# Kernel tuning notes

Hardware: AMD Instinct MI355X
Metric: run time of the kernel (lower is better)

The kernel has to match this reference:

```python
import jax, jax.numpy as jnp
import numpy as np

T = 10.0           # distillation temperature (init arg T)
LOSS_WEIGHT = 1.0  # module-level loss_weight (init arg)
EPS_STD = 1e-07
EPS_RATIO = 1e-08

ROWS, BINS = 1048576, 17  # (4*N, n+1), n = 16


def setup_inputs() -> dict:
    key = jax.random.key(0)
    k1, k2, k3 = jax.random.split(key, 3)
    pred = jax.random.normal(k1, (ROWS, BINS), dtype=jnp.float32)
    soft_label = jax.random.normal(k2, (ROWS, BINS), dtype=jnp.float32)
    weight = jax.random.uniform(k3, (ROWS,), dtype=jnp.float32)
    return {"pred": pred, "soft_label": soft_label, "weight": weight}


def _normalize(logit):
    # torch .std() is unbiased (ddof=1)
    mean = jnp.mean(logit, axis=-1, keepdims=True)
    stdv = jnp.std(logit, axis=-1, keepdims=True, ddof=1)
    return (logit - mean) / (EPS_STD + stdv)


def reference(pred, soft_label, weight):
    soft = jax.lax.stop_gradient(soft_label)  # detach_target=True

    # kd_loss_ls with logit_stand=True
    ls = _normalize(pred)
    lt = _normalize(soft)
    log_p_student = jax.nn.log_softmax(ls / T, axis=1)
    log_p_teacher = jax.nn.log_softmax(lt / T, axis=1)
    p_teacher = jnp.exp(log_p_teacher)
    # F.kl_div(log_pred, target, 'none') = target * (log(target) - log_pred)
    loss_ls = jnp.mean(jnp.sum(p_teacher * (log_p_teacher - log_p_student), axis=1)) * (T * T)

    # sum_distributions_loop on target = softmax(soft_label) -- batched full conv1d
    target = jax.nn.softmax(soft, axis=1)            # (4N, bins)
    n_rows, bins = target.shape
    N = n_rows // 4
    t = target.reshape(N, 4, bins)
    top, bottom, left, right = t[:, 0], t[:, 1], t[:, 2], t[:, 3]
    # pad+flip+conv1d in torch == true full convolution, length 2*bins-1 = 2n+1
    conv_full = jax.vmap(lambda a, b: jnp.convolve(a, b, mode='full'))
    sum_lr = conv_full(left, right)                   # (N, 2n+1)
    sum_tb = conv_full(top, bottom)                   # (N, 2n+1)
    target_ratio = sum_lr / (sum_tb + EPS_RATIO)

    # weighted_loss wrapper: loss * weight, then 'mean' reduction; outer * loss_weight
    loss = LOSS_WEIGHT * jnp.mean(loss_ls * weight)
    return loss, target_ratio
```

## Files before the change

kernel.cpp:

```cpp
#include <hip/hip_runtime.h>

#define ROWS 1048576
#define BINS 17
#define RPB 128
#define NBLK (ROWS / RPB)
#define NPART (2 * NBLK)
#define GPB (RPB / 4)
#define CONV_N 33
#define L2E 1.442695040888963f
#define LN2 0.6931471805599453f

template <bool PART>
__global__ __launch_bounds__(128, 4) void kd_main(
    const float* __restrict__ pred,
    const float* __restrict__ soft,
    const float* __restrict__ weight,
    float* __restrict__ out,
    float* __restrict__ ws)
{
    __shared__ float sA[RPB * BINS];
    __shared__ float sB[RPB * BINS];
    const int tid = threadIdx.x;
    const long long base = (long long)blockIdx.x * (RPB * BINS);

    const float4* p4 = reinterpret_cast<const float4*>(pred + base);
    const float4* q4 = reinterpret_cast<const float4*>(soft + base);
    float4* a4 = reinterpret_cast<float4*>(sA);
    float4* b4 = reinterpret_cast<float4*>(sB);
#pragma unroll
    for (int k = 0; k < 4; ++k) {
        a4[k * RPB + tid] = p4[k * RPB + tid];
        b4[k * RPB + tid] = q4[k * RPB + tid];
    }
    if (tid < 32) {
        a4[512 + tid] = p4[512 + tid];
        b4[512 + tid] = q4[512 + tid];
    }
    const float w = weight[blockIdx.x * RPB + tid];
    __syncthreads();

    float x[BINS], y[BINS];
    float sx = 0.f, sy = 0.f, sxx = 0.f, syy = 0.f;
    float xmx = -1e30f, ymx = -1e30f;
#pragma unroll
    for (int j = 0; j < BINS; ++j) {
        x[j] = sA[tid * BINS + j];
        y[j] = sB[tid * BINS + j];
        sx += x[j]; sxx = fmaf(x[j], x[j], sxx); xmx = fmaxf(xmx, x[j]);
        sy += y[j]; syy = fmaf(y[j], y[j], syy); ymx = fmaxf(ymx, y[j]);
    }
    const float mx = sx * (1.0f / BINS);
    const float my = sy * (1.0f / BINS);
    const float vx = fmaxf(fmaf(-sx, mx, sxx), 0.f) * (1.0f / (BINS - 1));
    const float vy = fmaxf(fmaf(-sy, my, syy), 0.f) * (1.0f / (BINS - 1));
    const float sxl = (0.1f * L2E) *
        __builtin_amdgcn_rcpf(1e-7f + __builtin_amdgcn_sqrtf(vx));
    const float syl = (0.1f * L2E) *
        __builtin_amdgcn_rcpf(1e-7f + __builtin_amdgcn_sqrtf(vy));
    const float cA = -xmx * sxl;
    const float cB = -ymx * syl;
    const float cT = -ymx * L2E;

    float et[BINS];
    float sea = 0.f, seb = 0.f, ts = 0.f, sdb = 0.f;
#pragma unroll
    for (int j = 0; j < BINS; ++j) {
        const float aj = fmaf(x[j], sxl, cA);
        const float bj = fmaf(y[j], syl, cB);
        const float ea = exp2f(aj);
        const float eb = exp2f(bj);
        const float tv = exp2f(fmaf(y[j], L2E, cT));
        sea += ea; seb += eb; ts += tv;
        sdb = fmaf(eb, bj - aj, sdb);
        et[j] = tv;
    }
    const float kl = LN2 * (sdb * __builtin_amdgcn_rcpf(seb)
                            + (__log2f(sea) - __log2f(seb)));
    const float invts = __builtin_amdgcn_rcpf(ts);

#pragma unroll
    for (int j = 0; j < BINS; ++j)
        sA[tid * BINS + j] = et[j] * invts;

    float k2 = kl, w2 = w;
#pragma unroll
    for (int off = 32; off >= 1; off >>= 1) {
        k2 += __shfl_down(k2, off, 64);
        w2 += __shfl_down(w2, off, 64);
    }
    if ((tid & 63) == 0) {
        const int wv = tid >> 6;
        if (PART) {
            ws[2 * blockIdx.x + wv]         = k2;
            ws[NPART + 2 * blockIdx.x + wv] = w2;
        } else {
            atomicAdd(&ws[0], k2);
            atomicAdd(&ws[1], w2);
        }
    }

    __syncthreads();

    float* sR = sB;

    if (tid < 64) {
        const int g = tid >> 1;
        const int R = 4 * g + ((tid & 1) ? 0 : 2);
        float f[2 * BINS];
        const float2* pr = reinterpret_cast<const float2*>(&sA[R * BINS]);
#pragma unroll
        for (int i = 0; i < BINS; ++i) {
            const float2 v = pr[i];
            f[2 * i] = v.x; f[2 * i + 1] = v.y;
        }
        float accv[CONV_N];
#pragma unroll
        for (int j = 0; j < CONV_N; ++j) accv[j] = 0.f;
#pragma unroll
        for (int k = 0; k < BINS; ++k)
#pragma unroll
            for (int m = 0; m < BINS; ++m)
                accv[k + m] = fmaf(f[k], f[BINS + m], accv[k + m]);

#pragma unroll
        for (int j = 0; j < CONV_N; ++j) {
            const float o = __shfl_down(accv[j], 1, 64);
            if ((tid & 1) == 0)
                sR[g * CONV_N + j] = accv[j] *
                    __builtin_amdgcn_rcpf(o + 1e-8f);
        }
    }
    __syncthreads();

    const long long ob = 1 + (long long)blockIdx.x * (GPB * CONV_N);
#pragma unroll
    for (int i = 0; i < 8; ++i)
        out[ob + i * RPB + tid] = sR[i * RPB + tid];
    if (tid < 32) out[ob + 1024 + tid] = sR[1024 + tid];
}

template <bool PART>
__global__ __launch_bounds__(1024) void kd_reduce(
    const float* __restrict__ ws, float* __restrict__ out)
{
    if (!PART) {
        if (threadIdx.x == 0)
            out[0] = 100.0f * (ws[0] * (1.0f / ROWS)) * (ws[1] * (1.0f / ROWS));
        return;
    }
    __shared__ float red[32];
    const int tid = threadIdx.x;
    const float4* k4 = reinterpret_cast<const float4*>(ws);
    const float4* w4 = reinterpret_cast<const float4*>(ws + NPART);
    float ks = 0.f, wsum = 0.f;
#pragma unroll
    for (int i = 0; i < 4; ++i) {
        const float4 a = k4[i * 1024 + tid];
        const float4 b = w4[i * 1024 + tid];
        ks += (a.x + a.y) + (a.z + a.w);
        wsum += (b.x + b.y) + (b.z + b.w);
    }
#pragma unroll
    for (int off = 32; off >= 1; off >>= 1) {
        ks += __shfl_down(ks, off, 64);
        wsum += __shfl_down(wsum, off, 64);
    }
    if ((tid & 63) == 0) {
        red[(tid >> 6) * 2 + 0] = ks;
        red[(tid >> 6) * 2 + 1] = wsum;
    }
    __syncthreads();
    if (tid == 0) {
        float K = 0.f, W = 0.f;
#pragma unroll
        for (int i = 0; i < 16; ++i) { K += red[2 * i]; W += red[2 * i + 1]; }
        out[0] = 100.0f * (K * (1.0f / ROWS)) * (W * (1.0f / ROWS));
    }
}

extern "C" void kernel_launch(void* const* d_in, const int* in_sizes, int n_in,
                              void* d_out, int out_size, void* d_ws, size_t ws_size,
                              hipStream_t stream)
{
    const float* pred   = (const float*)d_in[0];
    const float* soft   = (const float*)d_in[1];
    const float* weight = (const float*)d_in[2];
    float* out = (float*)d_out;
    float* ws  = (float*)d_ws;

    if (ws_size >= (size_t)(2 * NPART) * sizeof(float)) {
        kd_main<true><<<NBLK, RPB, 0, stream>>>(pred, soft, weight, out, ws);
        kd_reduce<true><<<1, 1024, 0, stream>>>(ws, out);
    } else {
        hipMemsetAsync(ws, 0, 2 * sizeof(float), stream);
        kd_main<false><<<NBLK, RPB, 0, stream>>>(pred, soft, weight, out, ws);
        kd_reduce<false><<<1, 1024, 0, stream>>>(ws, out);
    }
}
```

Baseline: 183.0 us.

## Load rows directly into registers, drop input LDS staging, raise occupancy

Each thread now reads its 17-float pred and soft rows straight from global memory into registers, replacing the block-wide float4 copy into two shared arrays and the barrier after it. LDS use drops to one array plus a per-row reciprocal slot, and the launch bound is raised to 8 blocks per CU. The softmax normalization of the teacher row is moved into the convolution phase through the stored reciprocal, and the output staging now reuses the same array. The aim is to cut LDS traffic and footprint and to allow more blocks per CU. The trade-off is that the per-thread loads are strided and only 4-byte aligned, so they may not vectorize or coalesce as well as the old float4 copy.

```diff
diff --git a/kernel.cpp b/kernel.cpp
--- a/kernel.cpp
+++ b/kernel.cpp
@@ -11,41 +11,31 @@
 #define LN2 0.6931471805599453f
 
 template <bool PART>
-__global__ __launch_bounds__(128, 4) void kd_main(
+__global__ __launch_bounds__(128, 8) void kd_main(
     const float* __restrict__ pred,
     const float* __restrict__ soft,
     const float* __restrict__ weight,
     float* __restrict__ out,
     float* __restrict__ ws)
 {
-    __shared__ float sA[RPB * BINS];
-    __shared__ float sB[RPB * BINS];
+    __shared__ float sA[RPB * BINS + RPB];
+    float* sI = sA + RPB * BINS;
     const int tid = threadIdx.x;
-    const long long base = (long long)blockIdx.x * (RPB * BINS);
 
-    const float4* p4 = reinterpret_cast<const float4*>(pred + base);
-    const float4* q4 = reinterpret_cast<const float4*>(soft + base);
-    float4* a4 = reinterpret_cast<float4*>(sA);
-    float4* b4 = reinterpret_cast<float4*>(sB);
+    const long long rowbase = ((long long)blockIdx.x * RPB + tid) * BINS;
+    const float* px = pred + rowbase;
+    const float* py = soft + rowbase;
+    float x[BINS], y[BINS];
 #pragma unroll
-    for (int k = 0; k < 4; ++k) {
-        a4[k * RPB + tid] = p4[k * RPB + tid];
-        b4[k * RPB + tid] = q4[k * RPB + tid];
-    }
-    if (tid < 32) {
-        a4[512 + tid] = p4[512 + tid];
-        b4[512 + tid] = q4[512 + tid];
-    }
+    for (int j = 0; j < BINS; ++j) x[j] = px[j];
+#pragma unroll
+    for (int j = 0; j < BINS; ++j) y[j] = py[j];
     const float w = weight[blockIdx.x * RPB + tid];
-    __syncthreads();
 
-    float x[BINS], y[BINS];
     float sx = 0.f, sy = 0.f, sxx = 0.f, syy = 0.f;
     float xmx = -1e30f, ymx = -1e30f;
 #pragma unroll
     for (int j = 0; j < BINS; ++j) {
-        x[j] = sA[tid * BINS + j];
-        y[j] = sB[tid * BINS + j];
         sx += x[j]; sxx = fmaf(x[j], x[j], sxx); xmx = fmaxf(xmx, x[j]);
         sy += y[j]; syy = fmaf(y[j], y[j], syy); ymx = fmaxf(ymx, y[j]);
     }
@@ -61,7 +51,6 @@
     const float cB = -ymx * syl;
     const float cT = -ymx * L2E;
 
-    float et[BINS];
     float sea = 0.f, seb = 0.f, ts = 0.f, sdb = 0.f;
 #pragma unroll
     for (int j = 0; j < BINS; ++j) {
@@ -72,15 +61,11 @@
         const float tv = exp2f(fmaf(y[j], L2E, cT));
         sea += ea; seb += eb; ts += tv;
         sdb = fmaf(eb, bj - aj, sdb);
-        et[j] = tv;
+        sA[tid * BINS + j] = tv;
     }
     const float kl = LN2 * (sdb * __builtin_amdgcn_rcpf(seb)
                             + (__log2f(sea) - __log2f(seb)));
-    const float invts = __builtin_amdgcn_rcpf(ts);
-
-#pragma unroll
-    for (int j = 0; j < BINS; ++j)
-        sA[tid * BINS + j] = et[j] * invts;
+    sI[tid] = __builtin_amdgcn_rcpf(ts);
 
     float k2 = kl, w2 = w;
 #pragma unroll
@@ -101,17 +86,19 @@
 
     __syncthreads();
 
-    float* sR = sB;
+    float* sR = sA;
 
     if (tid < 64) {
         const int g = tid >> 1;
         const int R = 4 * g + ((tid & 1) ? 0 : 2);
+        const float s0 = sI[R], s1 = sI[R + 1];
         float f[2 * BINS];
         const float2* pr = reinterpret_cast<const float2*>(&sA[R * BINS]);
 #pragma unroll
         for (int i = 0; i < BINS; ++i) {
             const float2 v = pr[i];
-            f[2 * i] = v.x; f[2 * i + 1] = v.y;
+            f[2 * i]     = v.x * (2 * i     < BINS ? s0 : s1);
+            f[2 * i + 1] = v.y * (2 * i + 1 < BINS ? s0 : s1);
         }
         float accv[CONV_N];
 #pragma unroll
```

New measurement: 181.8 us. No clear change (-0.7%).
